# Kernel tuning notes

Measured on AMD Instinct MI355X. Metric: run time of the kernel, lower is better.

Reference implementation:

```python
import jax, jax.numpy as jnp
import numpy as np

ALPHA = 0.2  # LeakyReLU negative slope

def setup_inputs() -> dict:
    key = jax.random.key(0)
    k1, k2, k3, k4 = jax.random.split(key, 4)
    N, F_in, F_out = 8192, 512, 64
    x = jax.random.normal(k1, (N, F_in), dtype=jnp.float32)
    adj = jax.random.randint(k2, (N, N), 0, 2, dtype=jnp.int32)
    # xavier-normal-ish init
    weight = jax.random.normal(k3, (F_in, F_out), dtype=jnp.float32) * np.sqrt(2.0 / (F_in + F_out))
    a = jax.random.normal(k4, (2 * F_out, 1), dtype=jnp.float32) * np.sqrt(2.0 / (2 * F_out + 1))
    return {"x": x, "adj": adj, "weight": weight, "a": a}

def reference(x, adj, weight, a):
    # Wh: [N, F_out]
    Wh = x @ weight
    F_out = weight.shape[1]
    a1 = a[:F_out, 0]   # applies to source (row) node
    a2 = a[F_out:, 0]   # applies to target (col) node
    # e[i,j] = LeakyReLU(Wh[i]@a1 + Wh[j]@a2)  -- broadcast-add instead of O(N^2*2F) concat
    s1 = Wh @ a1        # [N]
    s2 = Wh @ a2        # [N]
    e = s1[:, None] + s2[None, :]              # [N, N]
    e = jnp.where(e > 0, e, ALPHA * e)         # LeakyReLU
    e = jnp.where(adj > 0, e, jnp.float32(-9e15))
    attention = jax.nn.softmax(e, axis=1)      # [N, N]
    h_prime = attention @ Wh                   # [N, F_out]
    return jax.nn.elu(h_prime)                 # concat=True -> ELU
```

## Files before the change

kernel.cpp:

```cpp
#include <hip/hip_runtime.h>
#include <hip/hip_bf16.h>
#include <cstdint>
#include <cstddef>

#define N_NODES 8192
#define F_IN 512
#define F_OUT 64
#define LOG2E 1.44269504f

#define JSPLIT 8
#define JPB (N_NODES / JSPLIT)
#define JC 256
#define NCHUNK (JPB / JC)

typedef __attribute__((ext_vector_type(8))) short short8v;
typedef __attribute__((ext_vector_type(4))) float f32x4;
typedef __attribute__((ext_vector_type(4))) int i32x4;
typedef __attribute__((ext_vector_type(4))) unsigned int u32x4;

static __device__ __forceinline__ unsigned short f2bf(float f) {
    union { float f; unsigned u; } v; v.f = f;
    unsigned u = v.u + 0x7FFFu + ((v.u >> 16) & 1u);
    return (unsigned short)(u >> 16);
}
static __device__ __forceinline__ float bf2f(unsigned short b) {
    union { unsigned u; float f; } v; v.u = ((unsigned)b) << 16;
    return v.f;
}
static __device__ __forceinline__ unsigned cvt_pk_bf16(float lo, float hi) {
    unsigned r;
    asm("v_cvt_pk_bf16_f32 %0, %1, %2" : "=v"(r) : "v"(lo), "v"(hi));
    return r;
}


__global__ __launch_bounds__(256)
void gat_wconv(const float* __restrict__ W, unsigned short* __restrict__ whf,
               unsigned short* __restrict__ wlf) {
    const int t = blockIdx.x * 256 + threadIdx.x;
    const int tile = t >> 6, lane = t & 63;
    const int kt = tile >> 2, ct = tile & 3;
    const int k0 = kt * 32 + ((lane >> 4) << 3);
    const int c  = ct * 16 + (lane & 15);
    short8v h, l;
    #pragma unroll
    for (int i = 0; i < 8; ++i) {
        float v = W[(size_t)(k0 + i) * F_OUT + c];
        unsigned short hb = f2bf(v);
        h[i] = (short)hb;
        l[i] = (short)f2bf(v - bf2f(hb));
    }
    const size_t dst = (size_t)tile * 512 + (size_t)lane * 8;
    *(short8v*)(whf + dst) = h;
    *(short8v*)(wlf + dst) = l;
}

__global__ __launch_bounds__(256)
void gat_prep(const float* __restrict__ x, const unsigned short* __restrict__ whf,
              const unsigned short* __restrict__ wlf, const float* __restrict__ a,
              unsigned short* __restrict__ whtf,
              float* __restrict__ s1, float* __restrict__ s2) {
    __shared__ f32x4 red[2][4][64];
    __shared__ unsigned short ldsT[64][40];
    const int tid = threadIdx.x;
    const int lane = tid & 63;
    const int wv = tid >> 6;
    const int rt = wv & 1;
    const int kh = wv >> 1;
    const int l15 = lane & 15, g = lane >> 4;
    const int jt = blockIdx.x;
    const int row0 = jt * 32 + rt * 16;

    f32x4 acc[4] = {{0.f,0.f,0.f,0.f},{0.f,0.f,0.f,0.f},{0.f,0.f,0.f,0.f},{0.f,0.f,0.f,0.f}};

    const float* xp = x + (size_t)(row0 + l15) * F_IN + kh * 256 + g * 8;
    float4 v[16];
    #pragma unroll
    for (int q = 0; q < 8; ++q) {
        v[2 * q]     = *(const float4*)(xp + q * 32);
        v[2 * q + 1] = *(const float4*)(xp + q * 32 + 4);
    }
    #pragma unroll
    for (int q = 0; q < 8; ++q) {
        const int kt = kh * 8 + q;
        float vv[8] = {v[2*q].x, v[2*q].y, v[2*q].z, v[2*q].w,
                       v[2*q+1].x, v[2*q+1].y, v[2*q+1].z, v[2*q+1].w};
        short8v xh, xl;
        #pragma unroll
        for (int i = 0; i < 8; ++i) {
            unsigned short hb = f2bf(vv[i]);
            xh[i] = (short)hb;
            xl[i] = (short)f2bf(vv[i] - bf2f(hb));
        }
        const unsigned short* wp = whf + (size_t)(kt * 4) * 512 + (size_t)lane * 8;
        const unsigned short* lp = wlf + (size_t)(kt * 4) * 512 + (size_t)lane * 8;
        #pragma unroll
        for (int ct = 0; ct < 4; ++ct) {
            short8v wh = *(const short8v*)(wp + ct * 512);
            short8v wl = *(const short8v*)(lp + ct * 512);
            acc[ct] = __builtin_amdgcn_mfma_f32_16x16x32_bf16(xh, wh, acc[ct], 0, 0, 0);
            acc[ct] = __builtin_amdgcn_mfma_f32_16x16x32_bf16(xl, wh, acc[ct], 0, 0, 0);
            acc[ct] = __builtin_amdgcn_mfma_f32_16x16x32_bf16(xh, wl, acc[ct], 0, 0, 0);
        }
    }

    if (kh == 1) {
        #pragma unroll
        for (int ct = 0; ct < 4; ++ct) red[rt][ct][lane] = acc[ct];
    }
    __syncthreads();

    if (kh == 0) {
        #pragma unroll
        for (int ct = 0; ct < 4; ++ct) acc[ct] += red[rt][ct][lane];

        #pragma unroll
        for (int r = 0; r < 4; ++r) {
            float p1 = 0.f, p2 = 0.f;
            #pragma unroll
            for (int ct = 0; ct < 4; ++ct) {
                p1 = fmaf(acc[ct][r], a[ct * 16 + l15], p1);
                p2 = fmaf(acc[ct][r], a[64 + ct * 16 + l15], p2);
            }
            p1 += __shfl_xor(p1, 1); p2 += __shfl_xor(p2, 1);
            p1 += __shfl_xor(p1, 2); p2 += __shfl_xor(p2, 2);
            p1 += __shfl_xor(p1, 4); p2 += __shfl_xor(p2, 4);
            p1 += __shfl_xor(p1, 8); p2 += __shfl_xor(p2, 8);
            if (l15 == 0) {
                s1[row0 + g * 4 + r] = p1 * LOG2E;
                s2[row0 + g * 4 + r] = p2 * LOG2E;
            }
        }

        #pragma unroll
        for (int ct = 0; ct < 4; ++ct) {
            ushort4 pk;
            pk.x = f2bf(acc[ct][0]); pk.y = f2bf(acc[ct][1]);
            pk.z = f2bf(acc[ct][2]); pk.w = f2bf(acc[ct][3]);
            *(ushort4*)&ldsT[ct * 16 + l15][rt * 16 + g * 4] = pk;
        }
    }
    __syncthreads();

    {
        const int jb = jt >> 2, gj = jt & 3;
        const int m  = tid >> 6;
        const int ct = (tid >> 4) & 3;
        const int c  = tid & 15;
        short8v sv = *(const short8v*)&ldsT[ct * 16 + c][m * 8];
        *(short8v*)(whtf + (size_t)jb * 8192 + m * 2048 + ct * 512
                         + (size_t)(gj * 16 + c) * 8) = sv;
    }
}

__global__ __launch_bounds__(512, 4)
void gat_main(const int* __restrict__ adj, const unsigned short* __restrict__ whtf,
              const float* __restrict__ s1, const float* __restrict__ s2,
              float* __restrict__ numpart, float* __restrict__ denpart) {
    __shared__ unsigned short lds[2][JC * F_OUT];
    const int tid  = threadIdx.x;
    const int lane = tid & 63;
    const int wv   = tid >> 6;
    const int l15  = lane & 15, g = lane >> 4;
    const int rg   = blockIdx.x >> 3;
    const int js   = blockIdx.x & 7;
    const int rowbase = rg * 128 + wv * 16;
    const int row  = rowbase + l15;
    const int j0   = js * JPB;
    const float s1r = s1[row];

    const char* gbase = (const char*)whtf + (size_t)j0 * 128;
    const int*   abase = adj + (size_t)row * N_NODES + j0 + g * 32;
    const float* s2base = s2 + j0 + g * 32;

    f32x4 acc0 = {0.f, 0.f, 0.f, 0.f};
    f32x4 acc1 = acc0, acc2 = acc0, acc3 = acc0;
    float dsum = 0.f;

    #define STAGE(ch, buf) do { \
        const char* _g = gbase + (size_t)(ch) * 32768 + (size_t)tid * 16; \
        char* _l = (char*)&lds[buf][0] + (size_t)wv * 1024; \
        _Pragma("unroll") \
        for (int _i = 0; _i < 4; ++_i) \
            __builtin_amdgcn_global_load_lds( \
                (const __attribute__((address_space(1))) void*)(_g + _i * 8192), \
                (__attribute__((address_space(3))) void*)(_l + _i * 8192), 16, 0, 0); \
    } while (0)

    STAGE(0, 0);
    __syncthreads();

    for (int ch = 0; ch < NCHUNK; ++ch) {
        const int cur = ch & 1;
        if (ch < NCHUNK - 1) STAGE(ch + 1, cur ^ 1);

        const unsigned short* lbuf = &lds[cur][0];
        #pragma unroll
        for (int jb_l = 0; jb_l < 2; ++jb_l) {
            const int jg = ch * JC + jb_l * 128;
            i32x4 aj[8];
            #pragma unroll
            for (int q = 0; q < 8; ++q)
                aj[q] = *(const i32x4*)(abase + jg + q * 4);

            const unsigned short* gb = lbuf + jb_l * 8192;
            #pragma unroll
            for (int m = 0; m < 4; ++m) {
                float4 sa = *(const float4*)(s2base + jg + m * 8);
                float4 sb = *(const float4*)(s2base + jg + m * 8 + 4);

                short8v b0 = *(const short8v*)(gb + m * 2048 +   0 + lane * 8);
                short8v b1 = *(const short8v*)(gb + m * 2048 + 512 + lane * 8);
                short8v b2 = *(const short8v*)(gb + m * 2048 + 1024 + lane * 8);
                short8v b3 = *(const short8v*)(gb + m * 2048 + 1536 + lane * 8);

                float w0, w1, w2, w3, w4, w5, w6, w7;
                #define GAT_EL(wvar, ajv, s2v) do { \
                    float e = s1r + (s2v); e = fmaxf(e, 0.2f * e); \
                    float ex = __builtin_amdgcn_exp2f(e); \
                    wvar = ((ajv) > 0) ? ex : 0.f; dsum += wvar; } while (0);
                GAT_EL(w0, aj[2*m][0], sa.x) GAT_EL(w1, aj[2*m][1], sa.y)
                GAT_EL(w2, aj[2*m][2], sa.z) GAT_EL(w3, aj[2*m][3], sa.w)
                GAT_EL(w4, aj[2*m+1][0], sb.x) GAT_EL(w5, aj[2*m+1][1], sb.y)
                GAT_EL(w6, aj[2*m+1][2], sb.z) GAT_EL(w7, aj[2*m+1][3], sb.w)
                #undef GAT_EL

                u32x4 au;
                au[0] = cvt_pk_bf16(w0, w1);
                au[1] = cvt_pk_bf16(w2, w3);
                au[2] = cvt_pk_bf16(w4, w5);
                au[3] = cvt_pk_bf16(w6, w7);
                short8v afrag = __builtin_bit_cast(short8v, au);

                acc0 = __builtin_amdgcn_mfma_f32_16x16x32_bf16(afrag, b0, acc0, 0, 0, 0);
                acc1 = __builtin_amdgcn_mfma_f32_16x16x32_bf16(afrag, b1, acc1, 0, 0, 0);
                acc2 = __builtin_amdgcn_mfma_f32_16x16x32_bf16(afrag, b2, acc2, 0, 0, 0);
                acc3 = __builtin_amdgcn_mfma_f32_16x16x32_bf16(afrag, b3, acc3, 0, 0, 0);
            }
        }
        __syncthreads();
    }
    #undef STAGE

    dsum += __shfl_xor(dsum, 16);
    dsum += __shfl_xor(dsum, 32);
    if (lane < 16) denpart[(size_t)js * N_NODES + rowbase + lane] = dsum;

    float* np = numpart + ((size_t)js * N_NODES + rowbase) * F_OUT;
    #pragma unroll
    for (int r = 0; r < 4; ++r) {
        const int ro = (g * 4 + r) * F_OUT;
        np[ro +  0 + l15] = acc0[r];
        np[ro + 16 + l15] = acc1[r];
        np[ro + 32 + l15] = acc2[r];
        np[ro + 48 + l15] = acc3[r];
    }
}

__global__ __launch_bounds__(256)
void gat_combine(const float* __restrict__ numpart, const float* __restrict__ denpart,
                 float* __restrict__ out) {
    const int idx = blockIdx.x * 256 + threadIdx.x;
    const int r = idx >> 6;
    float num = 0.f, den = 0.f;
    #pragma unroll
    for (int c = 0; c < JSPLIT; ++c) {
        num += numpart[(size_t)c * N_NODES * F_OUT + idx];
        den += denpart[(size_t)c * N_NODES + r];
    }
    float h = num / den;
    out[idx] = h > 0.f ? h : __expf(h) - 1.f;
}

extern "C" void kernel_launch(void* const* d_in, const int* in_sizes, int n_in,
                              void* d_out, int out_size, void* d_ws, size_t ws_size,
                              hipStream_t stream) {
    const float* x      = (const float*)d_in[0];
    const int*   adj    = (const int*)d_in[1];
    const float* weight = (const float*)d_in[2];
    const float* a      = (const float*)d_in[3];
    float* out = (float*)d_out;

    char* ws = (char*)d_ws;
    unsigned short* whtf = (unsigned short*)ws;
    float* s1            = (float*)(ws + 1048576);
    float* s2            = (float*)(ws + 1048576 + 32768);
    unsigned short* whf  = (unsigned short*)(ws + 1048576 + 65536);
    unsigned short* wlf  = (unsigned short*)(ws + 1048576 + 131072);
    float* numpart       = (float*)(ws + 1048576 + 196608);
    float* denpart       = (float*)(ws + 1048576 + 196608 + (size_t)JSPLIT * N_NODES * F_OUT * 4);

    gat_wconv<<<16, 256, 0, stream>>>(weight, whf, wlf);
    gat_prep<<<N_NODES / 32, 256, 0, stream>>>(x, whf, wlf, a, whtf, s1, s2);
    gat_main<<<64 * JSPLIT, 512, 0, stream>>>(adj, whtf, s1, s2, numpart, denpart);
    gat_combine<<<N_NODES * F_OUT / 256, 256, 0, stream>>>(numpart, denpart, out);
}
```

Before: 91.07 us.

## Pack int32 adjacency into a bitmask before the attention kernel

Adds a pre-pass kernel that reads the int32 adjacency matrix and packs it into one bit per entry (8 MB instead of 256 MB). The main attention/MFMA kernel then reads a 32-bit mask word per lane group and tests bits, instead of streaming the int32 rows. This takes the large adjacency read out of the compute kernel and moves it into a purely streaming kernel, at the cost of an extra launch and an extra write and read of the mask. Packing uses `adj & 1` rather than `adj > 0`, which is only equivalent for 0/1 adjacency values.

```diff
diff --git a/kernel.cpp b/kernel.cpp
--- a/kernel.cpp
+++ b/kernel.cpp
@@ -33,6 +33,22 @@
     return r;
 }
 
+__global__ __launch_bounds__(256)
+void gat_pack(const int* __restrict__ adj, unsigned char* __restrict__ mask) {
+    const unsigned t = blockIdx.x * 256 + threadIdx.x;
+    const size_t stride = (size_t)2048 * 256;
+    #pragma unroll 4
+    for (int it = 0; it < 16; ++it) {
+        const size_t b = (size_t)it * stride + t;
+        const i32x4* p = (const i32x4*)(adj + b * 8);
+        i32x4 v0 = p[0], v1 = p[1];
+        unsigned byte =  (v0[0] & 1)        | ((v0[1] & 1) << 1)
+                      | ((v0[2] & 1) << 2)  | ((v0[3] & 1) << 3)
+                      | ((v1[0] & 1) << 4)  | ((v1[1] & 1) << 5)
+                      | ((v1[2] & 1) << 6)  | ((v1[3] & 1) << 7);
+        mask[b] = (unsigned char)byte;
+    }
+}
 
 __global__ __launch_bounds__(256)
 void gat_wconv(const float* __restrict__ W, unsigned short* __restrict__ whf,
@@ -154,7 +170,7 @@
 }
 
 __global__ __launch_bounds__(512, 4)
-void gat_main(const int* __restrict__ adj, const unsigned short* __restrict__ whtf,
+void gat_main(const unsigned char* __restrict__ mask, const unsigned short* __restrict__ whtf,
               const float* __restrict__ s1, const float* __restrict__ s2,
               float* __restrict__ numpart, float* __restrict__ denpart) {
     __shared__ unsigned short lds[2][JC * F_OUT];
@@ -170,8 +186,8 @@
     const float s1r = s1[row];
 
     const char* gbase = (const char*)whtf + (size_t)j0 * 128;
-    const int*   abase = adj + (size_t)row * N_NODES + j0 + g * 32;
-    const float* s2base = s2 + j0 + g * 32;
+    const unsigned* mrow = (const unsigned*)mask + (size_t)row * (N_NODES / 32) + (j0 >> 5) + g;
+    const float* s2b = s2 + j0 + g * 32;
 
     f32x4 acc0 = {0.f, 0.f, 0.f, 0.f};
     f32x4 acc1 = acc0, acc2 = acc0, acc3 = acc0;
@@ -196,33 +212,31 @@
 
         const unsigned short* lbuf = &lds[cur][0];
         #pragma unroll
-        for (int jb_l = 0; jb_l < 2; ++jb_l) {
-            const int jg = ch * JC + jb_l * 128;
-            i32x4 aj[8];
+        for (int h = 0; h < 2; ++h) {
+            const int jbl = ch * 2 + h;
+            const unsigned mw = mrow[jbl * 4];
+            const unsigned short* gb = lbuf + h * 8192;
             #pragma unroll
-            for (int q = 0; q < 8; ++q)
-                aj[q] = *(const i32x4*)(abase + jg + q * 4);
-
-            const unsigned short* gb = lbuf + jb_l * 8192;
-            #pragma unroll
-            for (int m = 0; m < 4; ++m) {
-                float4 sa = *(const float4*)(s2base + jg + m * 8);
-                float4 sb = *(const float4*)(s2base + jg + m * 8 + 4);
-
-                short8v b0 = *(const short8v*)(gb + m * 2048 +   0 + lane * 8);
-                short8v b1 = *(const short8v*)(gb + m * 2048 + 512 + lane * 8);
-                short8v b2 = *(const short8v*)(gb + m * 2048 + 1024 + lane * 8);
-                short8v b3 = *(const short8v*)(gb + m * 2048 + 1536 + lane * 8);
+            for (int q = 0; q < 4; ++q) {
+                const unsigned mb = (mw >> (q * 8)) & 0xffu;
+                const int jw = jbl * 128 + q * 8;
+                float4 sa = *(const float4*)(s2b + jw);
+                float4 sb = *(const float4*)(s2b + jw + 4);
+
+                short8v b0 = *(const short8v*)(gb + q * 2048 +    0 + lane * 8);
+                short8v b1 = *(const short8v*)(gb + q * 2048 +  512 + lane * 8);
+                short8v b2 = *(const short8v*)(gb + q * 2048 + 1024 + lane * 8);
+                short8v b3 = *(const short8v*)(gb + q * 2048 + 1536 + lane * 8);
 
                 float w0, w1, w2, w3, w4, w5, w6, w7;
-                #define GAT_EL(wvar, ajv, s2v) do { \
+                #define GAT_EL(wvar, bi, s2v) do { \
                     float e = s1r + (s2v); e = fmaxf(e, 0.2f * e); \
                     float ex = __builtin_amdgcn_exp2f(e); \
-                    wvar = ((ajv) > 0) ? ex : 0.f; dsum += wvar; } while (0);
-                GAT_EL(w0, aj[2*m][0], sa.x) GAT_EL(w1, aj[2*m][1], sa.y)
-                GAT_EL(w2, aj[2*m][2], sa.z) GAT_EL(w3, aj[2*m][3], sa.w)
-                GAT_EL(w4, aj[2*m+1][0], sb.x) GAT_EL(w5, aj[2*m+1][1], sb.y)
-                GAT_EL(w6, aj[2*m+1][2], sb.z) GAT_EL(w7, aj[2*m+1][3], sb.w)
+                    wvar = ((mb >> (bi)) & 1u) ? ex : 0.f; dsum += wvar; } while (0);
+                GAT_EL(w0, 0, sa.x) GAT_EL(w1, 1, sa.y)
+                GAT_EL(w2, 2, sa.z) GAT_EL(w3, 3, sa.w)
+                GAT_EL(w4, 4, sb.x) GAT_EL(w5, 5, sb.y)
+                GAT_EL(w6, 6, sb.z) GAT_EL(w7, 7, sb.w)
                 #undef GAT_EL
 
                 u32x4 au;
@@ -287,11 +301,13 @@
     float* s2            = (float*)(ws + 1048576 + 32768);
     unsigned short* whf  = (unsigned short*)(ws + 1048576 + 65536);
     unsigned short* wlf  = (unsigned short*)(ws + 1048576 + 131072);
-    float* numpart       = (float*)(ws + 1048576 + 196608);
-    float* denpart       = (float*)(ws + 1048576 + 196608 + (size_t)JSPLIT * N_NODES * F_OUT * 4);
-
+    float* numpart       = (float*)(ws + 1245184);
+    float* denpart       = (float*)(ws + 1245184 + 16777216);
+    unsigned char* mask  = (unsigned char*)(ws + 1245184 + 16777216 + 262144);
+
+    gat_pack<<<2048, 256, 0, stream>>>(adj, mask);
     gat_wconv<<<16, 256, 0, stream>>>(weight, whf, wlf);
     gat_prep<<<N_NODES / 32, 256, 0, stream>>>(x, whf, wlf, a, whtf, s1, s2);
-    gat_main<<<64 * JSPLIT, 512, 0, stream>>>(adj, whtf, s1, s2, numpart, denpart);
+    gat_main<<<64 * JSPLIT, 512, 0, stream>>>(mask, whtf, s1, s2, numpart, denpart);
     gat_combine<<<N_NODES * F_OUT / 256, 256, 0, stream>>>(numpart, denpart, out);
 }
```

Measured after the change: 100.7 us. 10.6% more time.
